# Performance work log

Hardware: AMD Instinct MI355X
Metric: run time of the kernel (lower is better)

Reference implementation:

```python
import jax, jax.numpy as jnp
import numpy as np

EPS = 1e-5
NEG_SLOPE = 0.01  # torch F.leaky_relu default


def _batchnorm(h, gamma, beta):
    # BatchNorm1d in training mode: batch stats over node dim, biased variance
    mu = jnp.mean(h, axis=0)
    var = jnp.mean((h - mu) ** 2, axis=0)
    return gamma * (h - mu) * jax.lax.rsqrt(var + EPS) + beta


def setup_inputs() -> dict:
    N, E, H, ED = 16384, 524288, 128, 16
    key = jax.random.key(0)
    ks = jax.random.split(key, 12)
    s = 1.0 / np.sqrt(H)
    return {
        "x": jax.random.normal(ks[0], (N, H), jnp.float32),
        "edge_index": jax.random.randint(ks[1], (2, E), 0, N, jnp.int64),
        "edge_attr": jax.random.normal(ks[2], (E, ED), jnp.float32),
        "Wq": jax.random.normal(ks[3], (H, H), jnp.float32) * s,
        "bq": jnp.zeros((H,), jnp.float32),
        "Wk": jax.random.normal(ks[4], (H, H), jnp.float32) * s,
        "bk": jnp.zeros((H,), jnp.float32),
        "Wv": jax.random.normal(ks[5], (H, H), jnp.float32) * s,
        "bv": jnp.zeros((H,), jnp.float32),
        "We": jax.random.normal(ks[6], (ED, 1), jnp.float32) * (1.0 / np.sqrt(ED)),
        "be": jnp.zeros((1,), jnp.float32),
        "bn1_g": jnp.ones((H,), jnp.float32),
        "bn1_b": jnp.zeros((H,), jnp.float32),
        "W1": jax.random.normal(ks[7], (H, 2 * H), jnp.float32) * s,
        "b1": jnp.zeros((2 * H,), jnp.float32),
        "W2": jax.random.normal(ks[8], (2 * H, H), jnp.float32) * (1.0 / np.sqrt(2 * H)),
        "b2": jnp.zeros((H,), jnp.float32),
        "bn2_g": jnp.ones((H,), jnp.float32),
        "bn2_b": jnp.zeros((H,), jnp.float32),
    }


def reference(x, edge_index, edge_attr, Wq, bq, Wk, bk, Wv, bv, We, be,
              bn1_g, bn1_b, W1, b1, W2, b2, bn2_g, bn2_b):
    N = x.shape[0]
    Q = x @ Wq + bq  # [N, H]
    K = x @ Wk + bk
    V = x @ Wv + bv
    Ebias = (edge_attr @ We + be)[:, 0]  # [E], num_heads == 1
    src, dst = edge_index[0], edge_index[1]
    # per-edge dot product over the FULL hidden dim (as in the source)
    scores = jnp.sum(Q[src] * K[dst], axis=1) + Ebias  # [E]
    scores = jnp.where(scores >= 0, scores, NEG_SLOPE * scores)
    # to_dense_adj scatter-adds edge_attr into a dense [N, N] adjacency
    adj = jnp.zeros((N, N), x.dtype).at[src, dst].add(scores)
    attn = jax.nn.softmax(adj, axis=1)  # dense softmax incl. zero non-edges
    x_new = attn @ V  # [N, H]
    h = _batchnorm(x + x_new, bn1_g, bn1_b)
    ffn = jax.nn.relu(h @ W1 + b1) @ W2 + b2
    return _batchnorm(h + ffn, bn2_g, bn2_b)
```

## Files before the change

### kernel.cpp

```cpp
#include <hip/hip_runtime.h>
#include <hip/hip_bf16.h>
#include <math.h>

#define H 128
#define H2 256
#define SLAB 96
#define LDA 136
#define LDA2 264
#define EPS 1e-5f

typedef __attribute__((ext_vector_type(8))) short s16x8;
typedef __attribute__((ext_vector_type(4))) float f32x4;

__device__ __forceinline__ unsigned short f2bf(float f) {
  unsigned u = __float_as_uint(f);
  unsigned r = (u + 0x7FFFu + ((u >> 16) & 1u)) >> 16;
  return (unsigned short)r;
}
__device__ __forceinline__ float bf2f(unsigned short s) {
  return __uint_as_float(((unsigned)s) << 16);
}

__global__ void wprep(const float* __restrict__ Wq, const float* __restrict__ Wk,
                      const float* __restrict__ Wv, const float* __restrict__ W1,
                      const float* __restrict__ W2,
                      short* qh, short* ql, short* kh, short* kl,
                      short* vh, short* w1h, short* w2h)
{
  int job = blockIdx.z;
  const float* src; short* dh; short* dl = nullptr; int Kd, Nn;
  if (job == 0)      { src = Wq; dh = qh;  dl = ql; Kd = 128; Nn = 128; }
  else if (job == 1) { src = Wk; dh = kh;  dl = kl; Kd = 128; Nn = 128; }
  else if (job == 2) { src = Wv; dh = vh;           Kd = 128; Nn = 128; }
  else if (job == 3) { src = W1; dh = w1h;          Kd = 128; Nn = 256; }
  else               { src = W2; dh = w2h;          Kd = 256; Nn = 128; }
  int t = blockIdx.x * 256 + threadIdx.x;
  if (t >= Kd * Nn) return;
  int n = t / Kd, k = t - n * Kd;
  float v = src[(size_t)k * Nn + n];
  unsigned short h = f2bf(v);
  dh[t] = (short)h;
  if (dl) dl[t] = (short)f2bf(v - bf2f(h));
}

__global__ __launch_bounds__(256) void qkv_mfma(
    const float* __restrict__ x,
    const short* __restrict__ Wqh, const short* __restrict__ Wql,
    const short* __restrict__ Wkh, const short* __restrict__ Wkl,
    const short* __restrict__ Wvh,
    const float* __restrict__ bq, const float* __restrict__ bk,
    const float* __restrict__ bv,
    float* __restrict__ Q, unsigned short* __restrict__ Kbf,
    unsigned short* __restrict__ Vbf, float* __restrict__ SV)
{
  __shared__ __align__(16) short Ahi[64 * LDA];
  __shared__ __align__(16) short Alo[64 * LDA];
  int tid = threadIdx.x;
  int bm = blockIdx.x * 64;
  int wave = tid >> 6, lane = tid & 63;
  int quad = lane >> 4, l16 = lane & 15;
  int wn = wave * 32;

#pragma unroll
  for (int i = 0; i < 4; ++i) {
    int g = i * 256 + tid;
    int row = g >> 4, f = g & 15;
    const float4* xp = (const float4*)&x[(size_t)(bm + row) * H + f * 8];
    float4 v0 = xp[0], v1 = xp[1];
    float vv[8] = {v0.x, v0.y, v0.z, v0.w, v1.x, v1.y, v1.z, v1.w};
    s16x8 hv, lv;
#pragma unroll
    for (int j = 0; j < 8; ++j) {
      unsigned short hh = f2bf(vv[j]);
      hv[j] = (short)hh;
      lv[j] = (short)f2bf(vv[j] - bf2f(hh));
    }
    *(s16x8*)&Ahi[row * LDA + f * 8] = hv;
    *(s16x8*)&Alo[row * LDA + f * 8] = lv;
  }
  __syncthreads();

  for (int ph = 0; ph < 3; ++ph) {
    const short* Bh = (ph == 0) ? Wqh : (ph == 1) ? Wkh : Wvh;
    const short* Bl = (ph == 0) ? Wql : (ph == 1) ? Wkl : nullptr;

    s16x8 bh[2][4], bl2[2][4];
#pragma unroll
    for (int nt = 0; nt < 2; ++nt)
#pragma unroll
      for (int ks = 0; ks < 4; ++ks)
        bh[nt][ks] = *(const s16x8*)&Bh[(size_t)(wn + nt * 16 + l16) * H + ks * 32 + quad * 8];
    if (Bl) {
#pragma unroll
      for (int nt = 0; nt < 2; ++nt)
#pragma unroll
        for (int ks = 0; ks < 4; ++ks)
          bl2[nt][ks] = *(const s16x8*)&Bl[(size_t)(wn + nt * 16 + l16) * H + ks * 32 + quad * 8];
    }

    f32x4 acc[4][2];
#pragma unroll
    for (int mt = 0; mt < 4; ++mt)
#pragma unroll
      for (int nt = 0; nt < 2; ++nt) acc[mt][nt] = (f32x4){0.f, 0.f, 0.f, 0.f};

#pragma unroll
    for (int ks = 0; ks < 4; ++ks) {
      int kof = ks * 32 + quad * 8;
      s16x8 ah[4], al[4];
#pragma unroll
      for (int mt = 0; mt < 4; ++mt) {
        ah[mt] = *(s16x8*)&Ahi[(mt * 16 + l16) * LDA + kof];
        al[mt] = *(s16x8*)&Alo[(mt * 16 + l16) * LDA + kof];
      }
#pragma unroll
      for (int mt = 0; mt < 4; ++mt)
#pragma unroll
        for (int nt = 0; nt < 2; ++nt) {
          acc[mt][nt] = __builtin_amdgcn_mfma_f32_16x16x32_bf16(ah[mt], bh[nt][ks], acc[mt][nt], 0, 0, 0);
          if (ph < 2) {
            acc[mt][nt] = __builtin_amdgcn_mfma_f32_16x16x32_bf16(ah[mt], bl2[nt][ks], acc[mt][nt], 0, 0, 0);
            acc[mt][nt] = __builtin_amdgcn_mfma_f32_16x16x32_bf16(al[mt], bh[nt][ks], acc[mt][nt], 0, 0, 0);
          }
        }
    }

    if (ph == 0) {
#pragma unroll
      for (int nt = 0; nt < 2; ++nt) {
        int col = wn + nt * 16 + l16;
        float bb = bq[col];
#pragma unroll
        for (int mt = 0; mt < 4; ++mt)
#pragma unroll
          for (int r = 0; r < 4; ++r) {
            int row = bm + mt * 16 + quad * 4 + r;
            Q[(size_t)row * H + col] = acc[mt][nt][r] + bb;
          }
      }
    } else if (ph == 1) {
#pragma unroll
      for (int nt = 0; nt < 2; ++nt) {
        int col = wn + nt * 16 + l16;
        float bb = bk[col];
#pragma unroll
        for (int mt = 0; mt < 4; ++mt)
#pragma unroll
          for (int r = 0; r < 4; ++r) {
            int row = bm + mt * 16 + quad * 4 + r;
            Kbf[(size_t)row * H + col] = f2bf(acc[mt][nt][r] + bb);
          }
      }
    } else {
#pragma unroll
      for (int nt = 0; nt < 2; ++nt) {
        int col = wn + nt * 16 + l16;
        float bb = bv[col];
        float ps = 0.f;
#pragma unroll
        for (int mt = 0; mt < 4; ++mt)
#pragma unroll
          for (int r = 0; r < 4; ++r) {
            int row = bm + mt * 16 + quad * 4 + r;
            float v = acc[mt][nt][r] + bb;
            Vbf[(size_t)row * H + col] = f2bf(v);
            ps += v;
          }
        ps += __shfl_xor(ps, 16);
        ps += __shfl_xor(ps, 32);
        if (quad == 0) atomicAdd(&SV[col], ps);
      }
    }
  }
}

__global__ __launch_bounds__(256) void ffn1_mfma(
    const float* __restrict__ h1, const short* __restrict__ W1h,
    const float* __restrict__ b1,
    const float* __restrict__ sum1, const float* __restrict__ sq1,
    const float* __restrict__ g1, const float* __restrict__ bb1,
    unsigned short* __restrict__ t1, float invN)
{
  __shared__ __align__(16) short As[64 * LDA];
  int tid = threadIdx.x;
  int bm = blockIdx.x * 64;
  int wave = tid >> 6, lane = tid & 63;
  int quad = lane >> 4, l16 = lane & 15;
  int wn = wave * 64;

  int f = tid & 15;
  float aP[8], bP[8];
#pragma unroll
  for (int j = 0; j < 8; ++j) {
    int c = f * 8 + j;
    float mu = sum1[c] * invN;
    float var = sq1[c] * invN - mu * mu;
    float rs = rsqrtf(var + EPS);
    float a = g1[c] * rs;
    aP[j] = a;
    bP[j] = bb1[c] - a * mu;
  }

#pragma unroll
  for (int i = 0; i < 4; ++i) {
    int g = i * 256 + tid;
    int row = g >> 4;
    const float4* xp = (const float4*)&h1[(size_t)(bm + row) * H + f * 8];
    float4 v0 = xp[0], v1 = xp[1];
    float vv[8] = {v0.x, v0.y, v0.z, v0.w, v1.x, v1.y, v1.z, v1.w};
    s16x8 hv;
#pragma unroll
    for (int j = 0; j < 8; ++j) hv[j] = (short)f2bf(aP[j] * vv[j] + bP[j]);
    *(s16x8*)&As[row * LDA + f * 8] = hv;
  }

  s16x8 bh[4][4];
#pragma unroll
  for (int nt = 0; nt < 4; ++nt)
#pragma unroll
    for (int ks = 0; ks < 4; ++ks)
      bh[nt][ks] = *(const s16x8*)&W1h[(size_t)(wn + nt * 16 + l16) * H + ks * 32 + quad * 8];
  __syncthreads();

  f32x4 acc[4][4];
#pragma unroll
  for (int mt = 0; mt < 4; ++mt)
#pragma unroll
    for (int nt = 0; nt < 4; ++nt) acc[mt][nt] = (f32x4){0.f, 0.f, 0.f, 0.f};

#pragma unroll
  for (int ks = 0; ks < 4; ++ks) {
    int kof = ks * 32 + quad * 8;
    s16x8 ah[4];
#pragma unroll
    for (int mt = 0; mt < 4; ++mt) ah[mt] = *(s16x8*)&As[(mt * 16 + l16) * LDA + kof];
#pragma unroll
    for (int mt = 0; mt < 4; ++mt)
#pragma unroll
      for (int nt = 0; nt < 4; ++nt)
        acc[mt][nt] = __builtin_amdgcn_mfma_f32_16x16x32_bf16(ah[mt], bh[nt][ks], acc[mt][nt], 0, 0, 0);
  }

#pragma unroll
  for (int nt = 0; nt < 4; ++nt) {
    int col = wn + nt * 16 + l16;
    float bb = b1[col];
#pragma unroll
    for (int mt = 0; mt < 4; ++mt)
#pragma unroll
      for (int r = 0; r < 4; ++r) {
        int row = bm + mt * 16 + quad * 4 + r;
        float v = acc[mt][nt][r] + bb;
        v = v > 0.f ? v : 0.f;
        t1[(size_t)row * H2 + col] = f2bf(v);
      }
  }
}

__global__ __launch_bounds__(256) void ffn2_mfma(
    const unsigned short* __restrict__ t1, const short* __restrict__ W2h,
    const float* __restrict__ b2, const float* __restrict__ h1,
    const float* __restrict__ sum1, const float* __restrict__ sq1,
    const float* __restrict__ g1, const float* __restrict__ bb1,
    float* __restrict__ h2, float* __restrict__ sum2, float* __restrict__ sq2,
    float invN)
{
  __shared__ __align__(16) short As[64 * LDA2];
  int tid = threadIdx.x;
  int bm = blockIdx.x * 64;
  int wave = tid >> 6, lane = tid & 63;
  int quad = lane >> 4, l16 = lane & 15;
  int wn = wave * 32;

#pragma unroll
  for (int i = 0; i < 8; ++i) {
    int g = i * 256 + tid;
    int row = g >> 5, f = g & 31;
    *(s16x8*)&As[row * LDA2 + f * 8] = *(const s16x8*)&t1[(size_t)(bm + row) * H2 + f * 8];
  }

  s16x8 bh[2][8];
#pragma unroll
  for (int nt = 0; nt < 2; ++nt)
#pragma unroll
    for (int ks = 0; ks < 8; ++ks)
      bh[nt][ks] = *(const s16x8*)&W2h[(size_t)(wn + nt * 16 + l16) * H2 + ks * 32 + quad * 8];
  __syncthreads();

  f32x4 acc[4][2];
#pragma unroll
  for (int mt = 0; mt < 4; ++mt)
#pragma unroll
    for (int nt = 0; nt < 2; ++nt) acc[mt][nt] = (f32x4){0.f, 0.f, 0.f, 0.f};

#pragma unroll
  for (int ks = 0; ks < 8; ++ks) {
    int kof = ks * 32 + quad * 8;
    s16x8 ah[4];
#pragma unroll
    for (int mt = 0; mt < 4; ++mt) ah[mt] = *(s16x8*)&As[(mt * 16 + l16) * LDA2 + kof];
#pragma unroll
    for (int mt = 0; mt < 4; ++mt)
#pragma unroll
      for (int nt = 0; nt < 2; ++nt)
        acc[mt][nt] = __builtin_amdgcn_mfma_f32_16x16x32_bf16(ah[mt], bh[nt][ks], acc[mt][nt], 0, 0, 0);
  }

#pragma unroll
  for (int nt = 0; nt < 2; ++nt) {
    int col = wn + nt * 16 + l16;
    float mu = sum1[col] * invN;
    float var = sq1[col] * invN - mu * mu;
    float rs = rsqrtf(var + EPS);
    float ra = g1[col] * rs;
    float rb = bb1[col] - ra * mu;
    float bb = b2[col];
    float ps = 0.f, pq = 0.f;
#pragma unroll
    for (int mt = 0; mt < 4; ++mt)
#pragma unroll
      for (int r = 0; r < 4; ++r) {
        int row = bm + mt * 16 + quad * 4 + r;
        float rr = ra * h1[(size_t)row * H + col] + rb;
        float v = acc[mt][nt][r] + bb + rr;
        h2[(size_t)row * H + col] = v;
        ps += v; pq += v * v;
      }
    ps += __shfl_xor(ps, 16); ps += __shfl_xor(ps, 32);
    pq += __shfl_xor(pq, 16); pq += __shfl_xor(pq, 32);
    if (quad == 0) {
      atomicAdd(&sum2[col], ps);
      atomicAdd(&sq2[col], pq);
    }
  }
}

__global__ void ebfill(const float* __restrict__ ea,
                       const float* __restrict__ We,
                       const float* __restrict__ be,
                       const int* __restrict__ ei,
                       int* __restrict__ cnt,
                       int2* __restrict__ slabDE, int E, int N)
{
  int grp = blockIdx.x & 7;
  int blk = blockIdx.x >> 3;
  int lo = grp * (N >> 3), hi = lo + (N >> 3);
  int per = E >> 8;
  int base = blk * per;
  float4 w0 = *(const float4*)&We[0], w1 = *(const float4*)&We[4];
  float4 w2 = *(const float4*)&We[8], w3 = *(const float4*)&We[12];
  float bias = be[0];
  for (int i = 0; i < per; i += 256) {
    int e = base + i + threadIdx.x;
    if (e >= E) continue;
    int src = ei[e];
    if (src < lo || src >= hi) continue;
    int dst = ei[E + e];
    const float4* p = (const float4*)&ea[(size_t)e * 16];
    float4 a0 = p[0], a1 = p[1], a2 = p[2], a3 = p[3];
    float s = a0.x * w0.x + a0.y * w0.y + a0.z * w0.z + a0.w * w0.w
            + a1.x * w1.x + a1.y * w1.y + a1.z * w1.z + a1.w * w1.w
            + a2.x * w2.x + a2.y * w2.y + a2.z * w2.z + a2.w * w2.w
            + a3.x * w3.x + a3.y * w3.y + a3.z * w3.z + a3.w * w3.w;
    s += bias;
    int pos = atomicAdd(&cnt[src], 1);
    if (pos < SLAB) {
      int2 rec; rec.x = dst; rec.y = __float_as_int(s);
      slabDE[src * SLAB + pos] = rec;
    }
  }
}

__global__ __launch_bounds__(256) void score_slab(
    const float* __restrict__ Q, const unsigned short* __restrict__ Kbf,
    const int* __restrict__ cnt, const int2* __restrict__ slabDE,
    float* __restrict__ sAslab, int N)
{
  int tid = threadIdx.x;
  int team = tid >> 3, sub = tid & 7;
  int local = team & 15;
  int i = blockIdx.x * 2 + (team >> 4);
  int k = cnt[i]; if (k > SLAB) k = SLAB;
  const float4* q4 = (const float4*)(Q + (size_t)i * H);
  float4 qa0 = q4[2 * sub], qa1 = q4[2 * sub + 1];
  float4 qb0 = q4[16 + 2 * sub], qb1 = q4[17 + 2 * sub];
  int base = i * SLAB;

  for (int p = local * 2; p < k; p += 32) {
    int2 de0 = slabDE[base + p];
    bool has1 = (p + 1 < k);
    int2 de1 = has1 ? slabDE[base + p + 1] : de0;
    const s16x8* k0 = (const s16x8*)(Kbf + (size_t)de0.x * H);
    const s16x8* k1 = (const s16x8*)(Kbf + (size_t)de1.x * H);
    s16x8 ka0 = k0[sub], kb0 = k0[8 + sub];
    s16x8 ka1 = k1[sub], kb1 = k1[8 + sub];
    float p0, p1;
    p0 = qa0.x * bf2f((unsigned short)ka0[0]) + qa0.y * bf2f((unsigned short)ka0[1])
       + qa0.z * bf2f((unsigned short)ka0[2]) + qa0.w * bf2f((unsigned short)ka0[3])
       + qa1.x * bf2f((unsigned short)ka0[4]) + qa1.y * bf2f((unsigned short)ka0[5])
       + qa1.z * bf2f((unsigned short)ka0[6]) + qa1.w * bf2f((unsigned short)ka0[7])
       + qb0.x * bf2f((unsigned short)kb0[0]) + qb0.y * bf2f((unsigned short)kb0[1])
       + qb0.z * bf2f((unsigned short)kb0[2]) + qb0.w * bf2f((unsigned short)kb0[3])
       + qb1.x * bf2f((unsigned short)kb0[4]) + qb1.y * bf2f((unsigned short)kb0[5])
       + qb1.z * bf2f((unsigned short)kb0[6]) + qb1.w * bf2f((unsigned short)kb0[7]);
    p1 = qa0.x * bf2f((unsigned short)ka1[0]) + qa0.y * bf2f((unsigned short)ka1[1])
       + qa0.z * bf2f((unsigned short)ka1[2]) + qa0.w * bf2f((unsigned short)ka1[3])
       + qa1.x * bf2f((unsigned short)ka1[4]) + qa1.y * bf2f((unsigned short)ka1[5])
       + qa1.z * bf2f((unsigned short)ka1[6]) + qa1.w * bf2f((unsigned short)ka1[7])
       + qb0.x * bf2f((unsigned short)kb1[0]) + qb0.y * bf2f((unsigned short)kb1[1])
       + qb0.z * bf2f((unsigned short)kb1[2]) + qb0.w * bf2f((unsigned short)kb1[3])
       + qb1.x * bf2f((unsigned short)kb1[4]) + qb1.y * bf2f((unsigned short)kb1[5])
       + qb1.z * bf2f((unsigned short)kb1[6]) + qb1.w * bf2f((unsigned short)kb1[7]);
    p0 += __shfl_xor(p0, 1); p1 += __shfl_xor(p1, 1);
    p0 += __shfl_xor(p0, 2); p1 += __shfl_xor(p1, 2);
    p0 += __shfl_xor(p0, 4); p1 += __shfl_xor(p1, 4);
    if (sub == 0) {
      float s0 = p0 + __int_as_float(de0.y);
      sAslab[base + p] = (s0 >= 0.f) ? s0 : 0.01f * s0;
      if (has1) {
        float s1 = p1 + __int_as_float(de1.y);
        sAslab[base + p + 1] = (s1 >= 0.f) ? s1 : 0.01f * s1;
      }
    }
  }
}

__global__ __launch_bounds__(256) void row_slab(
    const float* __restrict__ x, const unsigned short* __restrict__ Vbf,
    const float* __restrict__ SV, const int* __restrict__ cnt,
    const float* __restrict__ sAslab, const int2* __restrict__ slabDE,
    float* __restrict__ h1, int N)
{
  __shared__ float sv[8][SLAB];
  __shared__ int sd[8][SLAB];
  __shared__ unsigned char sown[8][SLAB];
  int team = threadIdx.x >> 5, lane = threadIdx.x & 31;
  int i = blockIdx.x * 8 + team;
  int k = cnt[i]; if (k > SLAB) k = SLAB;
  int base = i * SLAB;

  for (int p = lane; p < k; p += 32) {
    sv[team][p] = sAslab[base + p];
    sd[team][p] = slabDE[base + p].x;
  }
  __syncthreads();

  for (int p = lane; p < k; p += 32) {
    int d = sd[team][p], o = p;
    for (int q = 0; q < p; ++q)
      if (sd[team][q] == d) { o = q; break; }
    sown[team][p] = (unsigned char)o;
  }
  __syncthreads();
  for (int p = lane; p < k; p += 32)
    if (sown[team][p] != (unsigned char)p)
      atomicAdd(&sv[team][sown[team][p]], sv[team][p]);
  __syncthreads();

  float m = 0.f;
  for (int p = lane; p < k; p += 32)
    if (sown[team][p] == (unsigned char)p) m = fmaxf(m, sv[team][p]);
#pragma unroll
  for (int mask = 16; mask; mask >>= 1) m = fmaxf(m, __shfl_xor(m, mask));
  float em = expf(-m);

  float zl = 0.f;
  for (int p = lane; p < k; p += 32) {
    float cf = 0.f;
    if (sown[team][p] == (unsigned char)p) cf = expf(sv[team][p] - m) - em;
    sv[team][p] = cf;
    zl += cf;
  }
#pragma unroll
  for (int mask = 16; mask; mask >>= 1) zl += __shfl_xor(zl, mask);
  float Zi = 1.f / ((float)N * em + zl);
  __syncthreads();

  const ushort4* V4 = (const ushort4*)Vbf;
  float4 s4 = *(const float4*)&SV[lane * 4];
  float ax = em * s4.x, ay = em * s4.y, az = em * s4.z, aw = em * s4.w;
  int c = 0;
  for (; c + 8 <= k; c += 8) {
    float cf[8]; int dd[8]; ushort4 vv[8];
#pragma unroll
    for (int u = 0; u < 8; ++u) { cf[u] = sv[team][c + u]; dd[u] = sd[team][c + u]; }
#pragma unroll
    for (int u = 0; u < 8; ++u) vv[u] = V4[(size_t)dd[u] * 32 + lane];
#pragma unroll
    for (int u = 0; u < 8; ++u) {
      ax += cf[u] * bf2f(vv[u].x);
      ay += cf[u] * bf2f(vv[u].y);
      az += cf[u] * bf2f(vv[u].z);
      aw += cf[u] * bf2f(vv[u].w);
    }
  }
  for (; c < k; ++c) {
    float cf = sv[team][c];
    ushort4 v0 = V4[(size_t)sd[team][c] * 32 + lane];
    ax += cf * bf2f(v0.x); ay += cf * bf2f(v0.y);
    az += cf * bf2f(v0.z); aw += cf * bf2f(v0.w);
  }
  float4 xx = *(const float4*)&x[(size_t)i * H + lane * 4];
  float4 out;
  out.x = xx.x + ax * Zi; out.y = xx.y + ay * Zi;
  out.z = xx.z + az * Zi; out.w = xx.w + aw * Zi;
  *(float4*)&h1[(size_t)i * H + lane * 4] = out;
}

__global__ __launch_bounds__(128) void colstats(
    const float* __restrict__ X, float* __restrict__ sum,
    float* __restrict__ sumsq, int rowsPerBlock)
{
  int t = threadIdx.x;
  size_t r0 = (size_t)blockIdx.x * rowsPerBlock;
  float s = 0.f, ss = 0.f;
  for (int r = 0; r < rowsPerBlock; ++r) {
    float v = X[(r0 + r) * H + t];
    s += v; ss += v * v;
  }
  atomicAdd(&sum[t], s);
  atomicAdd(&sumsq[t], ss);
}

__global__ void bn_apply(const float* __restrict__ X,
                         const float* __restrict__ sum2, const float* __restrict__ sq2,
                         const float* __restrict__ g2, const float* __restrict__ bb2,
                         float* __restrict__ Y, size_t n4, float invN)
{
  size_t i = (size_t)blockIdx.x * blockDim.x + threadIdx.x;
  if (i >= n4) return;
  float4 v = ((const float4*)X)[i];
  int c = (int)((i * 4) & (H - 1));
  float4 s = *(const float4*)&sum2[c];
  float4 q = *(const float4*)&sq2[c];
  float4 g = *(const float4*)&g2[c];
  float4 b = *(const float4*)&bb2[c];
  float mu, var, rs, a;
  mu = s.x * invN; var = q.x * invN - mu * mu; rs = rsqrtf(var + EPS);
  a = g.x * rs; v.x = a * v.x + (b.x - a * mu);
  mu = s.y * invN; var = q.y * invN - mu * mu; rs = rsqrtf(var + EPS);
  a = g.y * rs; v.y = a * v.y + (b.y - a * mu);
  mu = s.z * invN; var = q.z * invN - mu * mu; rs = rsqrtf(var + EPS);
  a = g.z * rs; v.z = a * v.z + (b.z - a * mu);
  mu = s.w * invN; var = q.w * invN - mu * mu; rs = rsqrtf(var + EPS);
  a = g.w * rs; v.w = a * v.w + (b.w - a * mu);
  ((float4*)Y)[i] = v;
}

extern "C" void kernel_launch(void* const* d_in, const int* in_sizes, int n_in,
                              void* d_out, int out_size, void* d_ws, size_t ws_size,
                              hipStream_t stream)
{
  const float* x  = (const float*)d_in[0];
  const int*   ei = (const int*)d_in[1];
  const float* ea = (const float*)d_in[2];
  const float* Wq = (const float*)d_in[3];
  const float* bq = (const float*)d_in[4];
  const float* Wk = (const float*)d_in[5];
  const float* bk = (const float*)d_in[6];
  const float* Wv = (const float*)d_in[7];
  const float* bv = (const float*)d_in[8];
  const float* We = (const float*)d_in[9];
  const float* be = (const float*)d_in[10];
  const float* g1 = (const float*)d_in[11];
  const float* bb1 = (const float*)d_in[12];
  const float* W1 = (const float*)d_in[13];
  const float* b1 = (const float*)d_in[14];
  const float* W2 = (const float*)d_in[15];
  const float* b2 = (const float*)d_in[16];
  const float* g2 = (const float*)d_in[17];
  const float* bb2 = (const float*)d_in[18];

  int N = in_sizes[0] / H;
  int E = in_sizes[2] / 16;
  size_t NH = (size_t)N * H;
  float invN = 1.0f / (float)N;

  float* Q   = (float*)d_ws;
  float* KmSlot = Q + NH;
  float* h1  = KmSlot + NH;
  unsigned short* Vbf = (unsigned short*)(h1 + NH);
  int2*  slabDE = (int2*)(Vbf + NH);
  float* sAslab = (float*)(slabDE + (size_t)N * SLAB);
  int*   cnt    = (int*)(sAslab + (size_t)N * SLAB);
  float* stats  = (float*)(cnt + N);
  float* SV   = stats;
  float* sum1 = stats + H;
  float* sq1  = stats + 2 * H;
  float* sum2 = stats + 3 * H;
  float* sq2  = stats + 4 * H;
  short* wbuf = (short*)(stats + 9 * H + 4);
  short* Wqh = wbuf;
  short* Wql = Wqh + 16384;
  short* Wkh = Wql + 16384;
  short* Wkl = Wkh + 16384;
  short* Wvh = Wkl + 16384;
  short* W1h = Wvh + 16384;
  short* W2h = W1h + 32768;
  unsigned short* Kbf = (unsigned short*)KmSlot;
  unsigned short* t1 = (unsigned short*)Q;
  float* h2 = KmSlot;

  hipMemsetAsync(cnt, 0, (size_t)N * sizeof(int), stream);
  hipMemsetAsync(stats, 0, (size_t)5 * H * sizeof(float), stream);

  wprep<<<dim3(128, 1, 5), 256, 0, stream>>>(Wq, Wk, Wv, W1, W2,
      Wqh, Wql, Wkh, Wkl, Wvh, W1h, W2h);

  qkv_mfma<<<dim3(N / 64), 256, 0, stream>>>(
      x, Wqh, Wql, Wkh, Wkl, Wvh, bq, bk, bv, Q, Kbf, Vbf, SV);

  ebfill<<<dim3(2048), 256, 0, stream>>>(ea, We, be, ei, cnt, slabDE, E, N);
  score_slab<<<dim3(N / 2), 256, 0, stream>>>(Q, Kbf, cnt, slabDE, sAslab, N);
  row_slab<<<dim3(N / 8), 256, 0, stream>>>(x, Vbf, SV, cnt, sAslab, slabDE, h1, N);

  colstats<<<dim3(128), 128, 0, stream>>>(h1, sum1, sq1, N / 128);

  ffn1_mfma<<<dim3(N / 64), 256, 0, stream>>>(h1, W1h, b1, sum1, sq1, g1, bb1, t1, invN);
  ffn2_mfma<<<dim3(N / 64), 256, 0, stream>>>(t1, W2h, b2, h1, sum1, sq1, g1, bb1,
                                              h2, sum2, sq2, invN);

  bn_apply<<<dim3((int)((NH / 4 + 255) / 256)), 256, 0, stream>>>(
      h2, sum2, sq2, g2, bb2, (float*)d_out, NH / 4, invN);
}
```

Before: 262.6 us.

## Fuse edge-bias fill into QKV, column stats into row pass, and FFN layers

Appends the edge-bias slab fill as extra blocks of the QKV GEMM launch, so the two independent jobs share one launch and can overlap. Folds BN1 column statistics into the attention row kernel through shared-memory and then global atomics, which removes a separate colstats pass over h1. Merges FFN1 and FFN2 into one kernel that keeps the ReLU intermediate in LDS with 32-row tiles, so the bf16 t1 buffer is never written to or read from global memory. The costs are more atomics, a heterogeneous block mix inside one grid, and smaller tiles in the FFN, which means more blocks that each reload the weights.

```diff
diff --git a/kernel.cpp b/kernel.cpp
--- a/kernel.cpp
+++ b/kernel.cpp
@@ -43,7 +43,7 @@
   if (dl) dl[t] = (short)f2bf(v - bf2f(h));
 }
 
-__global__ __launch_bounds__(256) void qkv_mfma(
+__global__ __launch_bounds__(256) void qkv_eb(
     const float* __restrict__ x,
     const short* __restrict__ Wqh, const short* __restrict__ Wql,
     const short* __restrict__ Wkh, const short* __restrict__ Wkl,
@@ -51,11 +51,48 @@
     const float* __restrict__ bq, const float* __restrict__ bk,
     const float* __restrict__ bv,
     float* __restrict__ Q, unsigned short* __restrict__ Kbf,
-    unsigned short* __restrict__ Vbf, float* __restrict__ SV)
+    unsigned short* __restrict__ Vbf, float* __restrict__ SV,
+    const float* __restrict__ ea, const float* __restrict__ We,
+    const float* __restrict__ be, const int* __restrict__ ei,
+    int* __restrict__ cnt, int2* __restrict__ slabDE,
+    int E, int N, int QB)
 {
   __shared__ __align__(16) short Ahi[64 * LDA];
   __shared__ __align__(16) short Alo[64 * LDA];
   int tid = threadIdx.x;
+
+  if ((int)blockIdx.x >= QB) {
+    int b = blockIdx.x - QB;
+    int grp = b & 7;
+    int blk = b >> 3;
+    int lo = grp * (N >> 3), hi = lo + (N >> 3);
+    int per = E >> 8;
+    int base = blk * per;
+    float4 w0 = *(const float4*)&We[0], w1 = *(const float4*)&We[4];
+    float4 w2 = *(const float4*)&We[8], w3 = *(const float4*)&We[12];
+    float bias = be[0];
+    for (int i = 0; i < per; i += 256) {
+      int e = base + i + tid;
+      if (e >= E) continue;
+      int src = ei[e];
+      if (src < lo || src >= hi) continue;
+      int dst = ei[E + e];
+      const float4* p = (const float4*)&ea[(size_t)e * 16];
+      float4 a0 = p[0], a1 = p[1], a2 = p[2], a3 = p[3];
+      float s = a0.x * w0.x + a0.y * w0.y + a0.z * w0.z + a0.w * w0.w
+              + a1.x * w1.x + a1.y * w1.y + a1.z * w1.z + a1.w * w1.w
+              + a2.x * w2.x + a2.y * w2.y + a2.z * w2.z + a2.w * w2.w
+              + a3.x * w3.x + a3.y * w3.y + a3.z * w3.z + a3.w * w3.w;
+      s += bias;
+      int pos = atomicAdd(&cnt[src], 1);
+      if (pos < SLAB) {
+        int2 rec; rec.x = dst; rec.y = __float_as_int(s);
+        slabDE[src * SLAB + pos] = rec;
+      }
+    }
+    return;
+  }
+
   int bm = blockIdx.x * 64;
   int wave = tid >> 6, lane = tid & 63;
   int quad = lane >> 4, l16 = lane & 15;
@@ -174,19 +211,21 @@
   }
 }
 
-__global__ __launch_bounds__(256) void ffn1_mfma(
+__global__ __launch_bounds__(256) void ffn_fused(
     const float* __restrict__ h1, const short* __restrict__ W1h,
-    const float* __restrict__ b1,
+    const float* __restrict__ b1, const short* __restrict__ W2h,
+    const float* __restrict__ b2,
     const float* __restrict__ sum1, const float* __restrict__ sq1,
     const float* __restrict__ g1, const float* __restrict__ bb1,
-    unsigned short* __restrict__ t1, float invN)
+    float* __restrict__ h2, float* __restrict__ sum2, float* __restrict__ sq2,
+    float invN)
 {
-  __shared__ __align__(16) short As[64 * LDA];
+  __shared__ __align__(16) short As[32 * LDA];
+  __shared__ __align__(16) short Ts[32 * LDA2];
   int tid = threadIdx.x;
-  int bm = blockIdx.x * 64;
+  int bm = blockIdx.x * 32;
   int wave = tid >> 6, lane = tid & 63;
   int quad = lane >> 4, l16 = lane & 15;
-  int wn = wave * 64;
 
   int f = tid & 15;
   float aP[8], bP[8];
@@ -202,7 +241,7 @@
   }
 
 #pragma unroll
-  for (int i = 0; i < 4; ++i) {
+  for (int i = 0; i < 2; ++i) {
     int g = i * 256 + tid;
     int row = g >> 4;
     const float4* xp = (const float4*)&h1[(size_t)(bm + row) * H + f * 8];
@@ -214,101 +253,80 @@
     *(s16x8*)&As[row * LDA + f * 8] = hv;
   }
 
-  s16x8 bh[4][4];
+  int wn1 = wave * 64;
+  s16x8 b1f[4][4];
 #pragma unroll
   for (int nt = 0; nt < 4; ++nt)
 #pragma unroll
     for (int ks = 0; ks < 4; ++ks)
-      bh[nt][ks] = *(const s16x8*)&W1h[(size_t)(wn + nt * 16 + l16) * H + ks * 32 + quad * 8];
-  __syncthreads();
-
-  f32x4 acc[4][4];
-#pragma unroll
-  for (int mt = 0; mt < 4; ++mt)
-#pragma unroll
-    for (int nt = 0; nt < 4; ++nt) acc[mt][nt] = (f32x4){0.f, 0.f, 0.f, 0.f};
+      b1f[nt][ks] = *(const s16x8*)&W1h[(size_t)(wn1 + nt * 16 + l16) * H + ks * 32 + quad * 8];
+  __syncthreads();
+
+  f32x4 acc1[2][4];
+#pragma unroll
+  for (int mt = 0; mt < 2; ++mt)
+#pragma unroll
+    for (int nt = 0; nt < 4; ++nt) acc1[mt][nt] = (f32x4){0.f, 0.f, 0.f, 0.f};
 
 #pragma unroll
   for (int ks = 0; ks < 4; ++ks) {
     int kof = ks * 32 + quad * 8;
-    s16x8 ah[4];
-#pragma unroll
-    for (int mt = 0; mt < 4; ++mt) ah[mt] = *(s16x8*)&As[(mt * 16 + l16) * LDA + kof];
-#pragma unroll
-    for (int mt = 0; mt < 4; ++mt)
+    s16x8 ah[2];
+#pragma unroll
+    for (int mt = 0; mt < 2; ++mt) ah[mt] = *(s16x8*)&As[(mt * 16 + l16) * LDA + kof];
+#pragma unroll
+    for (int mt = 0; mt < 2; ++mt)
 #pragma unroll
       for (int nt = 0; nt < 4; ++nt)
-        acc[mt][nt] = __builtin_amdgcn_mfma_f32_16x16x32_bf16(ah[mt], bh[nt][ks], acc[mt][nt], 0, 0, 0);
+        acc1[mt][nt] = __builtin_amdgcn_mfma_f32_16x16x32_bf16(ah[mt], b1f[nt][ks], acc1[mt][nt], 0, 0, 0);
   }
 
 #pragma unroll
   for (int nt = 0; nt < 4; ++nt) {
-    int col = wn + nt * 16 + l16;
+    int col = wn1 + nt * 16 + l16;
     float bb = b1[col];
 #pragma unroll
-    for (int mt = 0; mt < 4; ++mt)
+    for (int mt = 0; mt < 2; ++mt)
 #pragma unroll
       for (int r = 0; r < 4; ++r) {
-        int row = bm + mt * 16 + quad * 4 + r;
-        float v = acc[mt][nt][r] + bb;
+        int row = mt * 16 + quad * 4 + r;
+        float v = acc1[mt][nt][r] + bb;
         v = v > 0.f ? v : 0.f;
-        t1[(size_t)row * H2 + col] = f2bf(v);
-      }
-  }
-}
-
-__global__ __launch_bounds__(256) void ffn2_mfma(
-    const unsigned short* __restrict__ t1, const short* __restrict__ W2h,
-    const float* __restrict__ b2, const float* __restrict__ h1,
-    const float* __restrict__ sum1, const float* __restrict__ sq1,
-    const float* __restrict__ g1, const float* __restrict__ bb1,
-    float* __restrict__ h2, float* __restrict__ sum2, float* __restrict__ sq2,
-    float invN)
-{
-  __shared__ __align__(16) short As[64 * LDA2];
-  int tid = threadIdx.x;
-  int bm = blockIdx.x * 64;
-  int wave = tid >> 6, lane = tid & 63;
-  int quad = lane >> 4, l16 = lane & 15;
-  int wn = wave * 32;
-
-#pragma unroll
-  for (int i = 0; i < 8; ++i) {
-    int g = i * 256 + tid;
-    int row = g >> 5, f = g & 31;
-    *(s16x8*)&As[row * LDA2 + f * 8] = *(const s16x8*)&t1[(size_t)(bm + row) * H2 + f * 8];
-  }
-
-  s16x8 bh[2][8];
+        Ts[row * LDA2 + col] = (short)f2bf(v);
+      }
+  }
+
+  int wn2 = wave * 32;
+  s16x8 b2f[2][8];
 #pragma unroll
   for (int nt = 0; nt < 2; ++nt)
 #pragma unroll
     for (int ks = 0; ks < 8; ++ks)
-      bh[nt][ks] = *(const s16x8*)&W2h[(size_t)(wn + nt * 16 + l16) * H2 + ks * 32 + quad * 8];
-  __syncthreads();
-
-  f32x4 acc[4][2];
-#pragma unroll
-  for (int mt = 0; mt < 4; ++mt)
-#pragma unroll
-    for (int nt = 0; nt < 2; ++nt) acc[mt][nt] = (f32x4){0.f, 0.f, 0.f, 0.f};
+      b2f[nt][ks] = *(const s16x8*)&W2h[(size_t)(wn2 + nt * 16 + l16) * H2 + ks * 32 + quad * 8];
+  __syncthreads();
+
+  f32x4 acc2[2][2];
+#pragma unroll
+  for (int mt = 0; mt < 2; ++mt)
+#pragma unroll
+    for (int nt = 0; nt < 2; ++nt) acc2[mt][nt] = (f32x4){0.f, 0.f, 0.f, 0.f};
 
 #pragma unroll
   for (int ks = 0; ks < 8; ++ks) {
     int kof = ks * 32 + quad * 8;
-    s16x8 ah[4];
-#pragma unroll
-    for (int mt = 0; mt < 4; ++mt) ah[mt] = *(s16x8*)&As[(mt * 16 + l16) * LDA2 + kof];
-#pragma unroll
-    for (int mt = 0; mt < 4; ++mt)
+    s16x8 ah[2];
+#pragma unroll
+    for (int mt = 0; mt < 2; ++mt) ah[mt] = *(s16x8*)&Ts[(mt * 16 + l16) * LDA2 + kof];
+#pragma unroll
+    for (int mt = 0; mt < 2; ++mt)
 #pragma unroll
       for (int nt = 0; nt < 2; ++nt)
-        acc[mt][nt] = __builtin_amdgcn_mfma_f32_16x16x32_bf16(ah[mt], bh[nt][ks], acc[mt][nt], 0, 0, 0);
+        acc2[mt][nt] = __builtin_amdgcn_mfma_f32_16x16x32_bf16(ah[mt], b2f[nt][ks], acc2[mt][nt], 0, 0, 0);
   }
 
 #pragma unroll
   for (int nt = 0; nt < 2; ++nt) {
-    int col = wn + nt * 16 + l16;
+    int col = wn2 + nt * 16 + l16;
     float mu = sum1[col] * invN;
     float var = sq1[col] * invN - mu * mu;
     float rs = rsqrtf(var + EPS);
@@ -317,12 +335,12 @@
     float bb = b2[col];
     float ps = 0.f, pq = 0.f;
 #pragma unroll
-    for (int mt = 0; mt < 4; ++mt)
+    for (int mt = 0; mt < 2; ++mt)
 #pragma unroll
       for (int r = 0; r < 4; ++r) {
         int row = bm + mt * 16 + quad * 4 + r;
         float rr = ra * h1[(size_t)row * H + col] + rb;
-        float v = acc[mt][nt][r] + bb + rr;
+        float v = acc2[mt][nt][r] + bb + rr;
         h2[(size_t)row * H + col] = v;
         ps += v; pq += v * v;
       }
@@ -331,42 +349,6 @@
     if (quad == 0) {
       atomicAdd(&sum2[col], ps);
       atomicAdd(&sq2[col], pq);
-    }
-  }
-}
-
-__global__ void ebfill(const float* __restrict__ ea,
-                       const float* __restrict__ We,
-                       const float* __restrict__ be,
-                       const int* __restrict__ ei,
-                       int* __restrict__ cnt,
-                       int2* __restrict__ slabDE, int E, int N)
-{
-  int grp = blockIdx.x & 7;
-  int blk = blockIdx.x >> 3;
-  int lo = grp * (N >> 3), hi = lo + (N >> 3);
-  int per = E >> 8;
-  int base = blk * per;
-  float4 w0 = *(const float4*)&We[0], w1 = *(const float4*)&We[4];
-  float4 w2 = *(const float4*)&We[8], w3 = *(const float4*)&We[12];
-  float bias = be[0];
-  for (int i = 0; i < per; i += 256) {
-    int e = base + i + threadIdx.x;
-    if (e >= E) continue;
-    int src = ei[e];
-    if (src < lo || src >= hi) continue;
-    int dst = ei[E + e];
-    const float4* p = (const float4*)&ea[(size_t)e * 16];
-    float4 a0 = p[0], a1 = p[1], a2 = p[2], a3 = p[3];
-    float s = a0.x * w0.x + a0.y * w0.y + a0.z * w0.z + a0.w * w0.w
-            + a1.x * w1.x + a1.y * w1.y + a1.z * w1.z + a1.w * w1.w
-            + a2.x * w2.x + a2.y * w2.y + a2.z * w2.z + a2.w * w2.w
-            + a3.x * w3.x + a3.y * w3.y + a3.z * w3.z + a3.w * w3.w;
-    s += bias;
-    int pos = atomicAdd(&cnt[src], 1);
-    if (pos < SLAB) {
-      int2 rec; rec.x = dst; rec.y = __float_as_int(s);
-      slabDE[src * SLAB + pos] = rec;
     }
   }
 }
@@ -429,15 +411,20 @@
     const float* __restrict__ x, const unsigned short* __restrict__ Vbf,
     const float* __restrict__ SV, const int* __restrict__ cnt,
     const float* __restrict__ sAslab, const int2* __restrict__ slabDE,
-    float* __restrict__ h1, int N)
+    float* __restrict__ h1, float* __restrict__ sum1, float* __restrict__ sq1,
+    int N)
 {
   __shared__ float sv[8][SLAB];
   __shared__ int sd[8][SLAB];
   __shared__ unsigned char sown[8][SLAB];
-  int team = threadIdx.x >> 5, lane = threadIdx.x & 31;
+  __shared__ float csum[H], csq[H];
+  int tid = threadIdx.x;
+  int team = tid >> 5, lane = tid & 31;
   int i = blockIdx.x * 8 + team;
   int k = cnt[i]; if (k > SLAB) k = SLAB;
   int base = i * SLAB;
+
+  if (tid < H) { csum[tid] = 0.f; csq[tid] = 0.f; }
 
   for (int p = lane; p < k; p += 32) {
     sv[team][p] = sAslab[base + p];
@@ -505,21 +492,17 @@
   out.x = xx.x + ax * Zi; out.y = xx.y + ay * Zi;
   out.z = xx.z + az * Zi; out.w = xx.w + aw * Zi;
   *(float4*)&h1[(size_t)i * H + lane * 4] = out;
-}
-
-__global__ __launch_bounds__(128) void colstats(
-    const float* __restrict__ X, float* __restrict__ sum,
-    float* __restrict__ sumsq, int rowsPerBlock)
-{
-  int t = threadIdx.x;
-  size_t r0 = (size_t)blockIdx.x * rowsPerBlock;
-  float s = 0.f, ss = 0.f;
-  for (int r = 0; r < rowsPerBlock; ++r) {
-    float v = X[(r0 + r) * H + t];
-    s += v; ss += v * v;
-  }
-  atomicAdd(&sum[t], s);
-  atomicAdd(&sumsq[t], ss);
+
+  int c0 = lane * 4;
+  atomicAdd(&csum[c0 + 0], out.x); atomicAdd(&csq[c0 + 0], out.x * out.x);
+  atomicAdd(&csum[c0 + 1], out.y); atomicAdd(&csq[c0 + 1], out.y * out.y);
+  atomicAdd(&csum[c0 + 2], out.z); atomicAdd(&csq[c0 + 2], out.z * out.z);
+  atomicAdd(&csum[c0 + 3], out.w); atomicAdd(&csq[c0 + 3], out.w * out.w);
+  __syncthreads();
+  if (tid < H) {
+    atomicAdd(&sum1[tid], csum[tid]);
+    atomicAdd(&sq1[tid], csq[tid]);
+  }
 }
 
 __global__ void bn_apply(const float* __restrict__ X,
@@ -598,7 +581,6 @@
   short* W1h = Wvh + 16384;
   short* W2h = W1h + 32768;
   unsigned short* Kbf = (unsigned short*)KmSlot;
-  unsigned short* t1 = (unsigned short*)Q;
   float* h2 = KmSlot;
 
   hipMemsetAsync(cnt, 0, (size_t)N * sizeof(int), stream);
@@ -607,18 +589,17 @@
   wprep<<<dim3(128, 1, 5), 256, 0, stream>>>(Wq, Wk, Wv, W1, W2,
       Wqh, Wql, Wkh, Wkl, Wvh, W1h, W2h);
 
-  qkv_mfma<<<dim3(N / 64), 256, 0, stream>>>(
-      x, Wqh, Wql, Wkh, Wkl, Wvh, bq, bk, bv, Q, Kbf, Vbf, SV);
-
-  ebfill<<<dim3(2048), 256, 0, stream>>>(ea, We, be, ei, cnt, slabDE, E, N);
+  int QB = N / 64;
+  qkv_eb<<<dim3(QB + 2048), 256, 0, stream>>>(
+      x, Wqh, Wql, Wkh, Wkl, Wvh, bq, bk, bv, Q, Kbf, Vbf, SV,
+      ea, We, be, ei, cnt, slabDE, E, N, QB);
+
   score_slab<<<dim3(N / 2), 256, 0, stream>>>(Q, Kbf, cnt, slabDE, sAslab, N);
-  row_slab<<<dim3(N / 8), 256, 0, stream>>>(x, Vbf, SV, cnt, sAslab, slabDE, h1, N);
-
-  colstats<<<dim3(128), 128, 0, stream>>>(h1, sum1, sq1, N / 128);
-
-  ffn1_mfma<<<dim3(N / 64), 256, 0, stream>>>(h1, W1h, b1, sum1, sq1, g1, bb1, t1, invN);
-  ffn2_mfma<<<dim3(N / 64), 256, 0, stream>>>(t1, W2h, b2, h1, sum1, sq1, g1, bb1,
-                                              h2, sum2, sq2, invN);
+  row_slab<<<dim3(N / 8), 256, 0, stream>>>(x, Vbf, SV, cnt, sAslab, slabDE,
+                                            h1, sum1, sq1, N);
+
+  ffn_fused<<<dim3(N / 32), 256, 0, stream>>>(h1, W1h, b1, W2h, b2,
+      sum1, sq1, g1, bb1, h2, sum2, sq2, invN);
 
   bn_apply<<<dim3((int)((NH / 4 + 255) / 256)), 256, 0, stream>>>(
       h2, sum2, sq2, g2, bb2, (float*)d_out, NH / 4, invN);
```

Result: slower. 291.7 us (+11.1%).
